# Kernel tuning notes

Measured on AMD Instinct MI355X. Metric: run time of the kernel, lower is better.

Reference implementation:

```python
import jax, jax.numpy as jnp
import numpy as np

N_ANCHORS = 250000
IMG_H, IMG_W = 1024, 1024
PRE_NMS = 6000    # num_pre_nms_test (inference path, training=False)
POST_NMS = 300    # num_post_nms_test
IOU_THR = 0.7


def setup_inputs() -> dict:
    key = jax.random.key(0)
    k1, k2, k3, k4, k5 = jax.random.split(key, 5)
    bboxes_txtytwth = jax.random.normal(k1, (N_ANCHORS, 4), dtype=jnp.float32) * 0.1
    # anchors as (ymin, xmin, ymax, xmax) scattered over the image
    cy = jax.random.uniform(k2, (N_ANCHORS,), dtype=jnp.float32) * IMG_H
    cx = jax.random.uniform(k3, (N_ANCHORS,), dtype=jnp.float32) * IMG_W
    ah = 32.0 + jax.random.uniform(k4, (N_ANCHORS,), dtype=jnp.float32) * 224.0
    aw = 32.0 + jax.random.uniform(k5, (N_ANCHORS,), dtype=jnp.float32) * 224.0
    anchors = jnp.stack([cy - 0.5 * ah, cx - 0.5 * aw,
                         cy + 0.5 * ah, cx + 0.5 * aw], axis=1)
    scores = jax.random.normal(jax.random.fold_in(key, 7), (N_ANCHORS,), dtype=jnp.float32)
    return {
        "bboxes_txtytwth": bboxes_txtytwth,
        "anchors": anchors,
        "scores": scores,
        "image_height": IMG_H,
        "image_width": IMG_W,
        "extractor_stride": 16,
    }


def _decode_bbox(anchors, deltas):
    # anchors: [N,4] (ymin,xmin,ymax,xmax); deltas: [N,4] (ty,tx,th,tw)
    h = anchors[:, 2] - anchors[:, 0]
    w = anchors[:, 3] - anchors[:, 1]
    cy = anchors[:, 0] + 0.5 * h
    cx = anchors[:, 1] + 0.5 * w
    ty, tx, th, tw = deltas[:, 0], deltas[:, 1], deltas[:, 2], deltas[:, 3]
    ncy = ty * h + cy
    ncx = tx * w + cx
    nh = jnp.exp(th) * h
    nw = jnp.exp(tw) * w
    return jnp.stack([ncy - 0.5 * nh, ncx - 0.5 * nw,
                      ncy + 0.5 * nh, ncx + 0.5 * nw], axis=1)


def _iou_matrix(b):
    # b: [K,4] -> [K,K] pairwise IoU
    area = (b[:, 2] - b[:, 0]) * (b[:, 3] - b[:, 1])
    iy = jnp.maximum(0.0, jnp.minimum(b[:, None, 2], b[None, :, 2]) -
                     jnp.maximum(b[:, None, 0], b[None, :, 0]))
    ix = jnp.maximum(0.0, jnp.minimum(b[:, None, 3], b[None, :, 3]) -
                     jnp.maximum(b[:, None, 1], b[None, :, 1]))
    inter = iy * ix
    return inter / (area[:, None] + area[None, :] - inter + 1e-9)


def _rpn_proposal(bboxes_txtytwth, anchors, scores, image_height, image_width,
                  extractor_stride):
    # 1) decode
    boxes = _decode_bbox(anchors, bboxes_txtytwth)
    # 2) clip to image + min-edge filter (filter implemented as score mask)
    ymin = jnp.clip(boxes[:, 0], 0.0, image_height)
    xmin = jnp.clip(boxes[:, 1], 0.0, image_width)
    ymax = jnp.clip(boxes[:, 2], 0.0, image_height)
    xmax = jnp.clip(boxes[:, 3], 0.0, image_width)
    boxes = jnp.stack([ymin, xmin, ymax, xmax], axis=1)
    valid = ((ymax - ymin) >= extractor_stride) & ((xmax - xmin) >= extractor_stride)
    masked_scores = jnp.where(valid, scores, -jnp.inf)
    # 3) pre-NMS top-k (sorted descending by score)
    top_scores, top_idx = jax.lax.top_k(masked_scores, PRE_NMS)
    top_boxes = boxes[top_idx]                      # [PRE_NMS,4]
    valid_k = jnp.isfinite(top_scores)
    # 4) greedy NMS over score-sorted boxes
    iou = _iou_matrix(top_boxes)                    # [PRE_NMS, PRE_NMS]
    order = jnp.arange(PRE_NMS)

    def body(i, suppressed):
        alive_i = jnp.logical_not(suppressed[i]) & valid_k[i]
        return suppressed | (alive_i & (iou[i] > IOU_THR) & (order > i))

    suppressed = jax.lax.fori_loop(0, PRE_NMS, body,
                                   jnp.zeros((PRE_NMS,), dtype=bool))
    keep = jnp.logical_not(suppressed) & valid_k
    # 5) first POST_NMS kept boxes (already score-ordered), fixed-shape output
    rank = jnp.cumsum(keep) - 1                     # position among kept
    tgt = jnp.where(keep & (rank < POST_NMS), rank, POST_NMS)
    out = jnp.zeros((POST_NMS + 1, 4), dtype=top_boxes.dtype).at[tgt].set(top_boxes)
    return out[:POST_NMS]                           # [POST_NMS,4], zero-padded


def reference(bboxes_txtytwth, anchors, scores, image_height, image_width,
              extractor_stride):
    return _rpn_proposal(bboxes_txtytwth, anchors, scores,
                         float(image_height), float(image_width),
                         float(extractor_stride))
```

## Files before the change

kernel.cpp:

```cpp
#include <hip/hip_runtime.h>

#pragma clang fp contract(off)

#define N_PRE   6000
#define N_POST  300
#define NW      94
#define SELCAP  7936
#define RS_BLK  124
#define NBIN    16384
#define DSHIFT  18
#define HPART   64

struct SelState {
    unsigned int thr;
};

__global__ void decode_kernel(const float4* __restrict__ deltas,
                              const float4* __restrict__ anchors,
                              const float*  __restrict__ scores,
                              const int* __restrict__ ph, const int* __restrict__ pw,
                              const int* __restrict__ ps,
                              unsigned int* __restrict__ s32out,
                              float4* __restrict__ boxes,
                              unsigned long long* __restrict__ sel,
                              unsigned long long* __restrict__ valid_words,
                              unsigned int* __restrict__ counter, int N)
{
#pragma clang fp contract(off)
    if (blockIdx.x == 0) {
        for (int t = threadIdx.x; t < SELCAP; t += 256) sel[t] = 0ull;
    } else if (blockIdx.x == 1) {
        if (threadIdx.x < 128) valid_words[threadIdx.x] = 0ull;
        if (threadIdx.x == 0) *counter = 0u;
    }
    int i = blockIdx.x * blockDim.x + threadIdx.x;
    if (i >= N) return;
    float H = (float)(*ph), W = (float)(*pw), S = (float)(*ps);
    float4 d = deltas[i];
    float4 a = anchors[i];
    float h = a.z - a.x, w = a.w - a.y;
    float cy = a.x + 0.5f * h, cx = a.y + 0.5f * w;
    float ncy = d.x * h + cy;
    float ncx = d.y * w + cx;
    float eh = (float)exp((double)d.z);
    float ew = (float)exp((double)d.w);
    float nh = eh * h;
    float nw = ew * w;
    float ymin = ncy - 0.5f * nh, xmin = ncx - 0.5f * nw;
    float ymax = ncy + 0.5f * nh, xmax = ncx + 0.5f * nw;
    ymin = fminf(fmaxf(ymin, 0.0f), H);
    xmin = fminf(fmaxf(xmin, 0.0f), W);
    ymax = fminf(fmaxf(ymax, 0.0f), H);
    xmax = fminf(fmaxf(xmax, 0.0f), W);
    bool valid = (ymax - ymin >= S) && (xmax - xmin >= S);
    float sc = scores[i];
    unsigned int bits = __float_as_uint(sc);
    unsigned int s32;
    if (!valid) s32 = 0x007FFFFFu;
    else        s32 = (bits & 0x80000000u) ? ~bits : (bits | 0x80000000u);
    s32out[i] = s32;
    boxes[i]  = make_float4(ymin, xmin, ymax, xmax);
}

__global__ __launch_bounds__(256) void hist_part(const unsigned int* __restrict__ s32in,
                                                 unsigned int* __restrict__ phist, int N)
{
    __shared__ unsigned int lh[NBIN];
    int tid = threadIdx.x;
    for (int j = tid; j < NBIN; j += 256) lh[j] = 0u;
    __syncthreads();
    for (int i = blockIdx.x * 256 + tid; i < N; i += HPART * 256)
        atomicAdd(&lh[s32in[i] >> DSHIFT], 1u);
    __syncthreads();
    unsigned int* dst = phist + blockIdx.x * NBIN;
    for (int j = tid; j < NBIN; j += 256) dst[j] = lh[j];
}

__global__ __launch_bounds__(256) void hist_reduce(const unsigned int* __restrict__ phist,
                                                   unsigned int* __restrict__ hist)
{
    int j = blockIdx.x * 256 + threadIdx.x;
    unsigned int s = 0;
#pragma unroll 8
    for (int b = 0; b < HPART; b++) s += phist[b * NBIN + j];
    hist[j] = s;
}

__global__ __launch_bounds__(1024) void pick_pass(const unsigned int* __restrict__ hist,
                                                  SelState* __restrict__ state)
{
    __shared__ unsigned int wsum[16];
    __shared__ int sel_chunk;
    __shared__ unsigned int sel_above;
    int tid = threadIdx.x, lane = tid & 63, wave = tid >> 6;
    const unsigned int k = 6000u;

    unsigned int s = 0;
    int base = tid * 16;
#pragma unroll
    for (int i = 0; i < 16; i++) s += hist[base + i];
    unsigned int S = s;
    for (int d = 1; d < 64; d <<= 1) {
        unsigned int t = __shfl_down(S, d);
        if (lane + d < 64) S += t;
    }
    if (lane == 0) wsum[wave] = S;
    __syncthreads();
    unsigned int above = 0;
    for (int w2 = wave + 1; w2 < 16; w2++) above += wsum[w2];
    unsigned int F  = S + above;
    unsigned int Fn = F - s;
    if (Fn < k && k <= F) { sel_chunk = tid; sel_above = Fn; }
    __syncthreads();
    int c = sel_chunk;
    unsigned int acc = sel_above;
    if (wave == 0 && lane < 16) {
        unsigned int b = hist[c * 16 + lane];
        unsigned int B = b;
        for (int d = 1; d < 16; d <<= 1) {
            unsigned int t = __shfl_down(B, d);
            if (lane + d < 16) B += t;
        }
        unsigned int Bn = B - b;
        unsigned int kk = k - acc;
        if (Bn < kk && kk <= B) state->thr = (unsigned int)(c * 16 + lane);
    }
}

__global__ void compact_kernel(const unsigned int* __restrict__ s32in,
                               const SelState* __restrict__ state,
                               unsigned long long* __restrict__ sel,
                               unsigned int* __restrict__ counter, int N)
{
    int i = blockIdx.x * blockDim.x + threadIdx.x;
    if (i >= N) return;
    unsigned int s32 = s32in[i];
    if ((s32 >> DSHIFT) >= state->thr) {
        unsigned int p = atomicAdd(counter, 1u);
        if (p < SELCAP)
            sel[p] = ((unsigned long long)s32 << 32) |
                     (unsigned long long)(~(unsigned int)i);
    }
}

__global__ __launch_bounds__(256) void rank_scatter(
    const unsigned long long* __restrict__ sel,
    const float4* __restrict__ boxes,
    float4* __restrict__ boxes_sorted,
    unsigned long long* __restrict__ valid_words, int N)
{
    __shared__ __align__(16) unsigned long long kbuf[SELCAP];
    __shared__ unsigned int cnt4[4][64];
    int tid = threadIdx.x;
    for (int t = tid; t < SELCAP; t += 256) kbuf[t] = sel[t];
    __syncthreads();
    int lane = tid & 63;
    int slice = tid >> 6;
    int i = blockIdx.x * 64 + lane;
    unsigned long long my = kbuf[i];
    const int SL = SELCAP / 4;
    int j0 = slice * SL;
    unsigned int c = 0;
#pragma unroll 8
    for (int j = j0; j < j0 + SL; j += 2) {
        ulonglong2 kk = *reinterpret_cast<const ulonglong2*>(&kbuf[j]);
        c += (kk.x > my) || (kk.x == my && j < i);
        c += (kk.y > my) || (kk.y == my && (j + 1) < i);
    }
    cnt4[slice][lane] = c;
    __syncthreads();
    if (tid < 64) {
        unsigned int rank = cnt4[0][tid] + cnt4[1][tid] + cnt4[2][tid] + cnt4[3][tid];
        unsigned long long key = kbuf[blockIdx.x * 64 + tid];
        if (key != 0ull && rank < N_PRE) {
            unsigned int s32 = (unsigned int)(key >> 32);
            unsigned int ii  = ~(unsigned int)(key & 0xFFFFFFFFull);
            float4 b = (ii < (unsigned int)N) ? boxes[ii] : make_float4(0.f,0.f,0.f,0.f);
            boxes_sorted[rank] = b;
            bool v = (s32 != 0x007FFFFFu) && (ii < (unsigned int)N);
            if (v) atomicOr(&valid_words[rank >> 6], 1ull << (rank & 63));
        }
    }
}

__global__ __launch_bounds__(64) void mask_kernel(const float4* __restrict__ boxes_sorted,
                                                  unsigned long long* __restrict__ mask)
{
#pragma clang fp contract(off)
    int rb = blockIdx.y, cb = blockIdx.x;
    if (cb < rb) return;
    __shared__ float4 cbox[64];
    int tid = threadIdx.x;
    int col0 = cb * 64;
    int c = col0 + tid;
    cbox[tid] = (c < N_PRE) ? boxes_sorted[c] : make_float4(0.f, 0.f, 0.f, 0.f);
    __syncthreads();
    int i = rb * 64 + tid;
    if (i >= N_PRE) return;
    float4 bi = boxes_sorted[i];
    float area_i = (bi.z - bi.x) * (bi.w - bi.y);
    unsigned long long word = 0ull;
#pragma unroll 8
    for (int j = 0; j < 64; j++) {
        float4 bj = cbox[j];
        float iy = fminf(bi.z, bj.z) - fmaxf(bi.x, bj.x);
        iy = fmaxf(iy, 0.0f);
        float ix = fminf(bi.w, bj.w) - fmaxf(bi.y, bj.y);
        ix = fmaxf(ix, 0.0f);
        float inter = iy * ix;
        float area_j = (bj.z - bj.x) * (bj.w - bj.y);
        float iou = inter / (((area_i + area_j) - inter) + 1e-9f);
        if ((col0 + j) > i && iou > 0.7f) word |= (1ull << j);
    }
    mask[(size_t)i * NW + cb] = word;
}

__global__ __launch_bounds__(64) void nms_seq(const unsigned long long* __restrict__ mask,
                                              const unsigned long long* __restrict__ valid_words,
                                              const float4* __restrict__ boxes_sorted,
                                              float* __restrict__ out)
{
#pragma clang fp contract(off)
    int lane = threadIdx.x;
    float4* out4 = reinterpret_cast<float4*>(out);

    for (int t = lane; t < N_POST; t += 64)
        out4[t] = make_float4(0.f, 0.f, 0.f, 0.f);

    unsigned long long rem0 = ~valid_words[lane];
    unsigned long long rem1 = ~((lane < NW - 64) ? valid_words[64 + lane] : 0ull);

    int rank = 0;
    float4 cb = boxes_sorted[lane];
    for (int w = 0; w < NW; w++) {
        float4 nb;
        if (w < NW - 1) nb = boxes_sorted[(w + 1) * 64 + lane];

        unsigned long long remw = (w < 64) ? __shfl(rem0, w) : __shfl(rem1, w - 64);
        unsigned long long aw = ~remw;

        unsigned long long keptb = 0ull;
        if (aw) {
            float area_me = (cb.z - cb.x) * (cb.w - cb.y);
            while (aw) {
                int b = __builtin_ctzll(aw);
                float kx = __shfl(cb.x, b);
                float ky = __shfl(cb.y, b);
                float kz = __shfl(cb.z, b);
                float kw = __shfl(cb.w, b);
                float iy = fmaxf(fminf(cb.z, kz) - fmaxf(cb.x, kx), 0.0f);
                float ix = fmaxf(fminf(cb.w, kw) - fmaxf(cb.y, ky), 0.0f);
                float inter = iy * ix;
                float ka = (kz - kx) * (kw - ky);
                float iou = inter / (((area_me + ka) - inter) + 1e-9f);
                unsigned long long sup = __ballot(iou > 0.7f);
                if (lane == b) out4[rank] = cb;
                keptb |= (1ull << b);
                rank++;
                aw &= ~(sup | (1ull << b));
                if (rank >= N_POST) break;
            }
        }

        if (rank >= N_POST) break;

        unsigned long long kb = keptb;
        while (kb) {
            int b0 = __builtin_ctzll(kb); kb &= kb - 1ull;
            int b1 = -1, b2 = -1, b3 = -1;
            if (kb) { b1 = __builtin_ctzll(kb); kb &= kb - 1ull; }
            if (kb) { b2 = __builtin_ctzll(kb); kb &= kb - 1ull; }
            if (kb) { b3 = __builtin_ctzll(kb); kb &= kb - 1ull; }
            const unsigned long long* p0 = mask + (size_t)(w * 64 + b0) * NW;
            unsigned long long l0 = p0[lane];
            unsigned long long h0 = (lane < NW - 64) ? p0[64 + lane] : 0ull;
            unsigned long long l1 = 0, h1 = 0, l2 = 0, h2 = 0, l3 = 0, h3 = 0;
            if (b1 >= 0) {
                const unsigned long long* p1 = mask + (size_t)(w * 64 + b1) * NW;
                l1 = p1[lane];
                h1 = (lane < NW - 64) ? p1[64 + lane] : 0ull;
            }
            if (b2 >= 0) {
                const unsigned long long* p2 = mask + (size_t)(w * 64 + b2) * NW;
                l2 = p2[lane];
                h2 = (lane < NW - 64) ? p2[64 + lane] : 0ull;
            }
            if (b3 >= 0) {
                const unsigned long long* p3 = mask + (size_t)(w * 64 + b3) * NW;
                l3 = p3[lane];
                h3 = (lane < NW - 64) ? p3[64 + lane] : 0ull;
            }
            rem0 |= (l0 | l1) | (l2 | l3);
            rem1 |= (h0 | h1) | (h2 | h3);
        }

        cb = nb;
    }
}

extern "C" void kernel_launch(void* const* d_in, const int* in_sizes, int n_in,
                              void* d_out, int out_size, void* d_ws, size_t ws_size,
                              hipStream_t stream)
{
    const float4* deltas  = (const float4*)d_in[0];
    const float4* anchors = (const float4*)d_in[1];
    const float*  scores  = (const float*)d_in[2];
    const int* ph = (const int*)d_in[3];
    const int* pw = (const int*)d_in[4];
    const int* ps = (const int*)d_in[5];
    int N = in_sizes[2];

    char* base = (char*)d_ws;
    size_t off = 0;
    auto alloc = [&](size_t sz) -> void* {
        void* p = base + off;
        off = (off + sz + 255) & ~(size_t)255;
        return p;
    };
    unsigned int* s32buf = (unsigned int*)alloc(sizeof(unsigned int) * (size_t)N);
    float4* boxes = (float4*)alloc(sizeof(float4) * (size_t)N);
    unsigned int* phist = (unsigned int*)alloc((size_t)HPART * NBIN * sizeof(unsigned int));
    unsigned int* hist = (unsigned int*)alloc(NBIN * sizeof(unsigned int));
    SelState* state = (SelState*)alloc(256);
    unsigned int* counter = (unsigned int*)alloc(256);
    unsigned long long* valid_words = (unsigned long long*)alloc(128 * 8);
    unsigned long long* sel = (unsigned long long*)alloc(sizeof(unsigned long long) * SELCAP);
    float4* boxes_sorted = (float4*)alloc(sizeof(float4) * 6016);
    unsigned long long* mask = (unsigned long long*)alloc(sizeof(unsigned long long) * (size_t)N_PRE * NW);

    int nb = (N + 255) / 256;
    decode_kernel<<<nb, 256, 0, stream>>>(deltas, anchors, scores, ph, pw, ps,
                                          s32buf, boxes, sel, valid_words, counter, N);
    hist_part<<<HPART, 256, 0, stream>>>(s32buf, phist, N);
    hist_reduce<<<NBIN / 256, 256, 0, stream>>>(phist, hist);
    pick_pass<<<1, 1024, 0, stream>>>(hist, state);
    compact_kernel<<<nb, 256, 0, stream>>>(s32buf, state, sel, counter, N);
    rank_scatter<<<RS_BLK, 256, 0, stream>>>(sel, boxes, boxes_sorted, valid_words, N);
    mask_kernel<<<dim3(NW, NW), 64, 0, stream>>>(boxes_sorted, mask);
    nms_seq<<<1, 64, 0, stream>>>(mask, valid_words, boxes_sorted, (float*)d_out);
}
```

Before: 290.6 us.

## Switch NMS suppression from push-style row ORs to pull-style per-word gather

The sequential NMS kernel no longer ORs each kept box's full mask row into a lane-distributed suppression bitmap after every word. Instead it records kept box indices in per-lane registers (up to 320 slots across five registers) and, for each word, gathers that word's column from every kept row, then reduces with xor-shuffles. This replaces the serial chain of dependent row loads after each word with one parallel gather-and-reduce per word. The cost is a 6-step shuffle reduction and scattered 8-byte loads on every word, even when no box is kept.

```diff
diff --git a/kernel.cpp b/kernel.cpp
--- a/kernel.cpp
+++ b/kernel.cpp
@@ -227,8 +227,10 @@
     for (int t = lane; t < N_POST; t += 64)
         out4[t] = make_float4(0.f, 0.f, 0.f, 0.f);
 
-    unsigned long long rem0 = ~valid_words[lane];
-    unsigned long long rem1 = ~((lane < NW - 64) ? valid_words[64 + lane] : 0ull);
+    unsigned long long vw0 = valid_words[lane];
+    unsigned long long vw1 = (lane < NW - 64) ? valid_words[64 + lane] : 0ull;
+
+    int s0 = -1, s1 = -1, s2 = -1, s3 = -1, s4 = -1;
 
     int rank = 0;
     float4 cb = boxes_sorted[lane];
@@ -236,10 +238,18 @@
         float4 nb;
         if (w < NW - 1) nb = boxes_sorted[(w + 1) * 64 + lane];
 
-        unsigned long long remw = (w < 64) ? __shfl(rem0, w) : __shfl(rem1, w - 64);
-        unsigned long long aw = ~remw;
-
-        unsigned long long keptb = 0ull;
+        unsigned long long m0 = 0, m1 = 0, m2 = 0, m3 = 0, m4 = 0;
+        if (s0 >= 0) m0 = mask[(size_t)s0 * NW + w];
+        if (s1 >= 0) m1 = mask[(size_t)s1 * NW + w];
+        if (s2 >= 0) m2 = mask[(size_t)s2 * NW + w];
+        if (s3 >= 0) m3 = mask[(size_t)s3 * NW + w];
+        if (s4 >= 0) m4 = mask[(size_t)s4 * NW + w];
+        unsigned long long m = (m0 | m1) | (m2 | m3) | m4;
+        for (int d = 1; d < 64; d <<= 1) m |= __shfl_xor(m, d);
+
+        unsigned long long vw = (w < 64) ? __shfl(vw0, w) : __shfl(vw1, w - 64);
+        unsigned long long aw = vw & ~m;
+
         if (aw) {
             float area_me = (cb.z - cb.x) * (cb.w - cb.y);
             while (aw) {
@@ -255,45 +265,22 @@
                 float iou = inter / (((area_me + ka) - inter) + 1e-9f);
                 unsigned long long sup = __ballot(iou > 0.7f);
                 if (lane == b) out4[rank] = cb;
-                keptb |= (1ull << b);
+                int idx = w * 64 + b;
+                if ((rank & 63) == lane) {
+                    switch (rank >> 6) {
+                        case 0: s0 = idx; break;
+                        case 1: s1 = idx; break;
+                        case 2: s2 = idx; break;
+                        case 3: s3 = idx; break;
+                        default: s4 = idx; break;
+                    }
+                }
                 rank++;
+                if (rank >= N_POST) break;
                 aw &= ~(sup | (1ull << b));
-                if (rank >= N_POST) break;
             }
         }
-
         if (rank >= N_POST) break;
-
-        unsigned long long kb = keptb;
-        while (kb) {
-            int b0 = __builtin_ctzll(kb); kb &= kb - 1ull;
-            int b1 = -1, b2 = -1, b3 = -1;
-            if (kb) { b1 = __builtin_ctzll(kb); kb &= kb - 1ull; }
-            if (kb) { b2 = __builtin_ctzll(kb); kb &= kb - 1ull; }
-            if (kb) { b3 = __builtin_ctzll(kb); kb &= kb - 1ull; }
-            const unsigned long long* p0 = mask + (size_t)(w * 64 + b0) * NW;
-            unsigned long long l0 = p0[lane];
-            unsigned long long h0 = (lane < NW - 64) ? p0[64 + lane] : 0ull;
-            unsigned long long l1 = 0, h1 = 0, l2 = 0, h2 = 0, l3 = 0, h3 = 0;
-            if (b1 >= 0) {
-                const unsigned long long* p1 = mask + (size_t)(w * 64 + b1) * NW;
-                l1 = p1[lane];
-                h1 = (lane < NW - 64) ? p1[64 + lane] : 0ull;
-            }
-            if (b2 >= 0) {
-                const unsigned long long* p2 = mask + (size_t)(w * 64 + b2) * NW;
-                l2 = p2[lane];
-                h2 = (lane < NW - 64) ? p2[64 + lane] : 0ull;
-            }
-            if (b3 >= 0) {
-                const unsigned long long* p3 = mask + (size_t)(w * 64 + b3) * NW;
-                l3 = p3[lane];
-                h3 = (lane < NW - 64) ? p3[64 + lane] : 0ull;
-            }
-            rem0 |= (l0 | l1) | (l2 | l3);
-            rem1 |= (h0 | h1) | (h2 | h3);
-        }
-
         cb = nb;
     }
 }
```

Measured after the change: 300.1 us. +3.3%, slower.
